# Performance work log

Measured on AMD Instinct MI355X. Metric: run time of the kernel, lower is better.

Reference implementation:

```python
import jax, jax.numpy as jnp
import numpy as np

N_NODES = 50000
N_EDGES = 1000000
IN_F = 128
OUT_F = 128
K = 4
NEG_SLOPE = 0.01  # torch nn.LeakyReLU() default
EPS = 1e-8


def setup_inputs() -> dict:
    key = jax.random.key(0)
    k1, k2, k3, k4, k5, k6 = jax.random.split(key, 6)
    x = jax.random.normal(k1, (N_NODES, IN_F), dtype=jnp.float32)
    e = jax.random.uniform(k2, (N_NODES, K), dtype=jnp.float32)
    stdv = 1.0 / np.sqrt(OUT_F)
    weights = jax.random.uniform(k3, (K, IN_F, OUT_F), minval=-stdv, maxval=stdv, dtype=jnp.float32)
    a = jax.random.normal(k4, (K, 2 * OUT_F, 1), dtype=jnp.float32) * 0.1
    # edge_index with no self-loops (remove_self_loops is then a no-op)
    row = jax.random.randint(k5, (N_EDGES,), 0, N_NODES)
    off = jax.random.randint(k6, (N_EDGES,), 1, N_NODES)
    col = (row + off) % N_NODES
    adj = jnp.stack([row, col]).astype(jnp.int64)
    return {"x": x, "e": e, "weights": weights, "a": a, "adj": adj}


def _canet_gat_forward(x, e, weights, a, adj):
    N = x.shape[0]
    out_f = weights.shape[-1]
    # add self loops (input has none)
    loops = jnp.arange(N, dtype=adj.dtype)
    src = jnp.concatenate([adj[0], loops])  # [Et]
    dst = jnp.concatenate([adj[1], loops])  # [Et]

    # per-head projection: [K, N, O]
    h = jnp.einsum('nd,kdo->kno', x, weights)

    # attention logits: a = [a_src; a_dst], logit_e = leakyrelu(h[src].a_src + h[dst].a_dst)
    a_src = a[:, :out_f, 0]   # [K, O]
    a_dst = a[:, out_f:, 0]   # [K, O]
    s_src = jnp.einsum('kno,ko->kn', h, a_src)  # [K, N]
    s_dst = jnp.einsum('kno,ko->kn', h, a_dst)  # [K, N]
    logits = s_src[:, src] + s_dst[:, dst]      # [K, Et]
    logits = jnp.where(logits >= 0, logits, NEG_SLOPE * logits)
    logits_max = jnp.max(logits, axis=1, keepdims=True)  # global max per head
    edge_e = jnp.exp(logits - logits_max)                # [K, Et]

    outputs = []
    for k in range(h.shape[0]):  # small fixed loop over heads (avoids [K,Et,O] blowup)
        denom = jax.ops.segment_sum(edge_e[k], src, num_segments=N) + EPS   # [N]
        msg = edge_e[k][:, None] * h[k][dst]                                # [Et, O]
        hi_k = jax.ops.segment_sum(msg, src, num_segments=N)                # [N, O]
        outputs.append(hi_k / denom[:, None])
    outputs = jnp.stack(outputs, axis=1)  # [N, K, O]

    out = jnp.sum(e[:, :, None] * outputs, axis=1)  # [N, O]
    return out + x  # residual (in_features == out_features)


def reference(x, e, weights, a, adj):
    return _canet_gat_forward(x, e, weights, a, adj)
```

## Files before the change

### kernel.cpp

```cpp
#include <hip/hip_runtime.h>
#include <hip/hip_bf16.h>
#include <cstddef>

#define NN 50000
#define NE 1000000
#define F  128
#define KH 4
#define NEG 0.01f
#define EPSF 1e-8f
#define CAP 64
#define NBIN 196
#define BINCAP 8192
#define EPB 4096
#define NB1 ((NE + EPB - 1) / EPB)
#define NBW 256
#define NBP 2048
#define STR (NBP * 4)
#define MXSTR 32

typedef short bf16x8 __attribute__((ext_vector_type(8)));
typedef float f32x4 __attribute__((ext_vector_type(4)));

__device__ inline ushort f2bf(float f) {
    __hip_bfloat16 b = __float2bfloat16(f);
    return *reinterpret_cast<ushort*>(&b);
}
__device__ inline float2 bf2_to_f2(unsigned int v) {
    union { unsigned int u; float f; } a, b;
    a.u = (v & 0xffffu) << 16;
    b.u = v & 0xffff0000u;
    return make_float2(a.f, b.f);
}
__device__ inline unsigned int packbf(float xl, float xh) {
    return (unsigned int)f2bf(xl) | ((unsigned int)f2bf(xh) << 16);
}
__device__ inline float lk(float v) { return (v >= 0.f) ? v : NEG * v; }

__global__ __launch_bounds__(256) void bin_kernel(const int* __restrict__ adj,
                                                  int* __restrict__ binTail,
                                                  unsigned int* __restrict__ binbuf,
                                                  const float* __restrict__ W,
                                                  const float* __restrict__ a,
                                                  ushort* __restrict__ wt,
                                                  float* __restrict__ vvg) {
    int b = blockIdx.x;
    int tid = threadIdx.x;
    if (b < NB1) {
        __shared__ int hist[NBIN];
        __shared__ int rpos[NBIN];
        int base = b * EPB;
        int nloc = min(EPB, NE - base);
        for (int i = tid; i < NBIN; i += 256) hist[i] = 0;
        __syncthreads();
        unsigned int pk[16];
#pragma unroll
        for (int u = 0; u < 16; u++) {
            int off = u * 256 + tid;
            if (off < nloc) {
                int e = base + off;
                unsigned int s = (unsigned int)adj[e];
                unsigned int d = (unsigned int)adj[NE + e];
                pk[u] = (s << 16) | d;
                atomicAdd(&hist[s >> 8], 1);
            } else pk[u] = 0xffffffffu;
        }
        __syncthreads();
        for (int i = tid; i < NBIN; i += 256) rpos[i] = atomicAdd(&binTail[i], hist[i]);
        __syncthreads();
#pragma unroll
        for (int u = 0; u < 16; u++) {
            if (pk[u] != 0xffffffffu) {
                int bn = pk[u] >> 24;
                int p = atomicAdd(&rpos[bn], 1);
                if (p < BINCAP) binbuf[(size_t)bn * BINCAP + p] = pk[u];
            }
        }
    } else if (b < NB1 + NBW) {
        int i = (b - NB1) * 256 + tid;
        int k = i >> 14;
        int dd = (i >> 7) & 127;
        int o = i & 127;
        wt[((size_t)k * F + o) * F + dd] = f2bf(W[i]);
    } else {
        int j0 = tid * 4;
#pragma unroll
        for (int ii = 0; ii < 4; ii++) {
            int j = j0 + ii;
            int side = j >> 9;
            int k = (j >> 7) & 3;
            int dd = j & 127;
            const float4* Wr = (const float4*)(W + (size_t)k * F * F + (size_t)dd * F);
            const float4* ar = (const float4*)(a + (size_t)k * 2 * F + side * F);
            float acc = 0.f;
#pragma unroll 8
            for (int o = 0; o < F / 4; o++) {
                float4 wv = Wr[o], av = ar[o];
                acc += wv.x * av.x + wv.y * av.y + wv.z * av.z + wv.w * av.w;
            }
            vvg[j] = acc;
        }
    }
}

__global__ __launch_bounds__(256) void build_prep_kernel(const int* __restrict__ binTail,
                                                         const unsigned int* __restrict__ binbuf,
                                                         int* __restrict__ cnt,
                                                         ushort* __restrict__ bucket16,
                                                         const float* __restrict__ vvg,
                                                         const float* __restrict__ x,
                                                         unsigned int* __restrict__ xb2,
                                                         float* __restrict__ ssrc4,
                                                         float* __restrict__ sdst4,
                                                         int* __restrict__ mxsi) {
    int tid = threadIdx.x;
    __shared__ __align__(16) int shmem[1024];
    __shared__ float bmax_s[4][8];

    if (blockIdx.x < NBIN) {
        int b = blockIdx.x;
        int* lcnt = shmem;
        int* lpos = shmem + 256;
        lcnt[tid] = 0;
        lpos[tid] = 0;
        __syncthreads();
        int tail = min(binTail[b], BINCAP);
        const unsigned int* bb = binbuf + (size_t)b * BINCAP;
        for (int i = tid; i < tail; i += 256) {
            unsigned int pk = bb[i];
            atomicAdd(&lcnt[(pk >> 16) & 255], 1);
        }
        __syncthreads();
        int n0 = b << 8;
        cnt[n0 + tid] = lcnt[tid];
        for (int i = tid; i < tail; i += 256) {
            unsigned int pk = bb[i];
            int sl = (pk >> 16) & 255;
            int p = atomicAdd(&lpos[sl], 1);
            if (p < CAP) bucket16[(size_t)(n0 + sl) * CAP + p] = (ushort)(pk & 0xffffu);
        }
        return;
    }

    float* vvf = (float*)shmem;
    ((float4*)vvf)[tid] = ((const float4*)vvg)[tid];
    __syncthreads();

    int wv = tid >> 6, lane = tid & 63;
    int gw = (blockIdx.x - NBIN) * 4 + wv;
    const float2* x2 = (const float2*)x;
    float2 vs[4], vd[4];
#pragma unroll
    for (int k = 0; k < 4; k++) {
        vs[k] = *(const float2*)&vvf[k * F + 2 * lane];
        vd[k] = *(const float2*)&vvf[(4 + k) * F + 2 * lane];
    }
    int l1 = lane & 1, l2 = lane & 2, l4 = lane & 4;
    int j = 4 * l1 + l2 + (l4 >> 2);
    float* sp = (j < 4) ? (ssrc4 + j) : (sdst4 + (j - 4));
    float mxv = 0.f;

    for (int n = gw; n < NN; n += 2 * STR) {
        int nb = n + STR;
        bool vb = nb < NN;
        float2 xa = x2[(size_t)n * 64 + lane];
        float2 xbv = vb ? x2[(size_t)nb * 64 + lane] : make_float2(0.f, 0.f);
        xb2[(size_t)n * 64 + lane] = packbf(xa.x, xa.y);
        if (vb) xb2[(size_t)nb * 64 + lane] = packbf(xbv.x, xbv.y);
        float s[8], q[8];
#pragma unroll
        for (int k = 0; k < 4; k++) {
            s[k]     = xa.x * vs[k].x + xa.y * vs[k].y;
            s[4 + k] = xa.x * vd[k].x + xa.y * vd[k].y;
            q[k]     = xbv.x * vs[k].x + xbv.y * vs[k].y;
            q[4 + k] = xbv.x * vd[k].x + xbv.y * vd[k].y;
        }
        float tA[4], tB[4];
#pragma unroll
        for (int i = 0; i < 4; i++) {
            float mA = l1 ? s[4 + i] : s[i];
            float oA = __shfl_xor(l1 ? s[i] : s[4 + i], 1);
            tA[i] = mA + oA;
            float mB = l1 ? q[4 + i] : q[i];
            float oB = __shfl_xor(l1 ? q[i] : q[4 + i], 1);
            tB[i] = mB + oB;
        }
        float uA[2], uB[2];
#pragma unroll
        for (int i = 0; i < 2; i++) {
            float mA = l2 ? tA[2 + i] : tA[i];
            float oA = __shfl_xor(l2 ? tA[i] : tA[2 + i], 2);
            uA[i] = mA + oA;
            float mB = l2 ? tB[2 + i] : tB[i];
            float oB = __shfl_xor(l2 ? tB[i] : tB[2 + i], 2);
            uB[i] = mB + oB;
        }
        float vA, vB;
        {
            float mA = l4 ? uA[1] : uA[0];
            float oA = __shfl_xor(l4 ? uA[0] : uA[1], 4);
            vA = mA + oA;
            float mB = l4 ? uB[1] : uB[0];
            float oB = __shfl_xor(l4 ? uB[0] : uB[1], 4);
            vB = mB + oB;
        }
        vA += __shfl_xor(vA, 8);  vB += __shfl_xor(vB, 8);
        vA += __shfl_xor(vA, 16); vB += __shfl_xor(vB, 16);
        vA += __shfl_xor(vA, 32); vB += __shfl_xor(vB, 32);
        if (lane < 8) {
            sp[(size_t)n * 4] = vA;
            if (vb) sp[(size_t)nb * 4] = vB;
        }
        mxv = fmaxf(mxv, fmaxf(vA, vB));
    }
    if (lane < 8) bmax_s[wv][j] = mxv;
    __syncthreads();
    if (tid < 8) {
        float m = fmaxf(fmaxf(bmax_s[0][tid], bmax_s[1][tid]),
                        fmaxf(bmax_s[2][tid], bmax_s[3][tid]));
        atomicMax(&mxsi[tid * MXSTR], __float_as_int(m));
    }
}

__global__ __launch_bounds__(256) void aggregate_kernel(const unsigned int* __restrict__ xb2,
                                                        const float* __restrict__ ssrc4,
                                                        const float* __restrict__ sdst4,
                                                        const float* __restrict__ mxs,
                                                        const int* __restrict__ cnt,
                                                        const ushort* __restrict__ bucket16,
                                                        const float* __restrict__ ew,
                                                        unsigned int* __restrict__ z2) {
    int wv = threadIdx.x >> 6, lane = threadIdx.x & 63;
    int n = blockIdx.x * 4 + wv;
    if (n >= NN) return;

    __shared__ int dsh[4][64];
    __shared__ __align__(16) float wsh[4][64][4];

    float m0 = lk(mxs[0 * MXSTR] + mxs[4 * MXSTR]);
    float m1 = lk(mxs[1 * MXSTR] + mxs[5 * MXSTR]);
    float m2 = lk(mxs[2 * MXSTR] + mxs[6 * MXSTR]);
    float m3 = lk(mxs[3 * MXSTR] + mxs[7 * MXSTR]);
    float4 ss  = *(const float4*)&ssrc4[(size_t)n * 4];
    float4 sdn = *(const float4*)&sdst4[(size_t)n * 4];
    float w0s = __expf(lk(ss.x + sdn.x) - m0);
    float w1s = __expf(lk(ss.y + sdn.y) - m1);
    float w2s = __expf(lk(ss.z + sdn.z) - m2);
    float w3s = __expf(lk(ss.w + sdn.w) - m3);

    int deg = min(cnt[n], CAP);
    if (lane < deg) {
        int d = (int)bucket16[(size_t)n * CAP + lane];
        dsh[wv][lane] = d;
        float4 sd = *(const float4*)&sdst4[(size_t)d * 4];
        float4 w;
        w.x = __expf(lk(ss.x + sd.x) - m0);
        w.y = __expf(lk(ss.y + sd.y) - m1);
        w.z = __expf(lk(ss.z + sd.z) - m2);
        w.w = __expf(lk(ss.w + sd.w) - m3);
        *(float4*)&wsh[wv][lane][0] = w;
    }

    float a0[4], a1[4], den[4];
    {
        float2 f = bf2_to_f2(xb2[(size_t)n * 64 + lane]);
        a0[0] = w0s * f.x; a1[0] = w0s * f.y; den[0] = w0s;
        a0[1] = w1s * f.x; a1[1] = w1s * f.y; den[1] = w1s;
        a0[2] = w2s * f.x; a1[2] = w2s * f.y; den[2] = w2s;
        a0[3] = w3s * f.x; a1[3] = w3s * f.y; den[3] = w3s;
    }

    for (int i = 0; i < deg; i += 8) {
        int du[8]; float4 wu[8]; unsigned int vu[8];
#pragma unroll
        for (int u = 0; u < 8; u++) {
            int iu = i + u;
            bool val = iu < deg;
            int sel = val ? iu : 0;
            du[u] = dsh[wv][sel];
            float4 w = *(const float4*)&wsh[wv][sel][0];
            wu[u] = val ? w : make_float4(0.f, 0.f, 0.f, 0.f);
        }
#pragma unroll
        for (int u = 0; u < 8; u++) vu[u] = xb2[(size_t)du[u] * 64 + lane];
#pragma unroll
        for (int u = 0; u < 8; u++) {
            float2 f = bf2_to_f2(vu[u]);
            float4 w = wu[u];
            a0[0] += w.x * f.x; a1[0] += w.x * f.y; den[0] += w.x;
            a0[1] += w.y * f.x; a1[1] += w.y * f.y; den[1] += w.y;
            a0[2] += w.z * f.x; a1[2] += w.z * f.y; den[2] += w.z;
            a0[3] += w.w * f.x; a1[3] += w.w * f.y; den[3] += w.w;
        }
    }

    float4 e4 = *(const float4*)&ew[(size_t)n * 4];
    float i0 = e4.x / (den[0] + EPSF);
    float i1 = e4.y / (den[1] + EPSF);
    float i2 = e4.z / (den[2] + EPSF);
    float i3 = e4.w / (den[3] + EPSF);
    size_t zb = (size_t)n * 256;
    z2[zb +   0 + lane] = packbf(a0[0] * i0, a1[0] * i0);
    z2[zb +  64 + lane] = packbf(a0[1] * i1, a1[1] * i1);
    z2[zb + 128 + lane] = packbf(a0[2] * i2, a1[2] * i2);
    z2[zb + 192 + lane] = packbf(a0[3] * i3, a1[3] * i3);
}

#define MT 64
__global__ __launch_bounds__(256) void gemm2_kernel(const ushort* __restrict__ z,
                                                    const ushort* __restrict__ wt,
                                                    const float* __restrict__ x,
                                                    float* __restrict__ out) {
    int row0 = blockIdx.x * MT;
    int tid = threadIdx.x;
    int wave = tid >> 6, lane = tid & 63;
    int quad = lane >> 4, l16 = lane & 15;
    __shared__ ushort ws[F][136];

    int arow = row0 + wave * 16 + l16;
    if (arow >= NN) arow = NN - 1;

    f32x4 acc[8];
#pragma unroll
    for (int i = 0; i < 8; i++) acc[i] = (f32x4){0.f, 0.f, 0.f, 0.f};

    for (int k = 0; k < KH; k++) {
        __syncthreads();
        const ushort* wk = wt + (size_t)k * F * F;
        for (int i = tid; i < F * 16; i += 256) {
            int r = i >> 4, c = (i & 15) * 8;
            *(uint4*)&ws[r][c] = *(const uint4*)&wk[r * F + c];
        }
        __syncthreads();
#pragma unroll
        for (int kt = 0; kt < 4; kt++) {
            int kb = kt * 32 + quad * 8;
            bf16x8 af = *(const bf16x8*)&z[(size_t)arow * 512 + k * F + kb];
#pragma unroll
            for (int ni = 0; ni < 8; ni++) {
                bf16x8 bf = *(const bf16x8*)&ws[ni * 16 + l16][kb];
                acc[ni] = __builtin_amdgcn_mfma_f32_16x16x32_bf16(af, bf, acc[ni], 0, 0, 0);
            }
        }
    }
#pragma unroll
    for (int r = 0; r < 4; r++) {
        int n = row0 + wave * 16 + quad * 4 + r;
        if (n < NN) {
#pragma unroll
            for (int ni = 0; ni < 8; ni++) {
                int o = ni * 16 + l16;
                out[(size_t)n * F + o] = x[(size_t)n * F + o] + acc[ni][r];
            }
        }
    }
}

extern "C" void kernel_launch(void* const* d_in, const int* in_sizes, int n_in,
                              void* d_out, int out_size, void* d_ws, size_t ws_size,
                              hipStream_t stream) {
    const float* x = (const float*)d_in[0];
    const float* e = (const float*)d_in[1];
    const float* W = (const float*)d_in[2];
    const float* a = (const float*)d_in[3];
    const int*   adj = (const int*)d_in[4];
    float* out = (float*)d_out;

    char* ws = (char*)d_ws;
    auto take = [&](size_t bytes) {
        char* p = ws;
        ws += (bytes + 255) & ~(size_t)255;
        return p;
    };
    ushort* z      = (ushort*)take((size_t)NN * KH * F * sizeof(ushort));
    unsigned int* xb2 = (unsigned int*)take((size_t)NN * F * sizeof(ushort));
    ushort* wt     = (ushort*)take((size_t)KH * F * F * sizeof(ushort));
    float* ssrc4   = (float*)take((size_t)NN * 4 * sizeof(float));
    float* sdst4   = (float*)take((size_t)NN * 4 * sizeof(float));
    int*   cnt     = (int*)take((size_t)NBIN * 256 * sizeof(int));
    ushort* bucket16 = (ushort*)take((size_t)NBIN * 256 * CAP * sizeof(ushort));
    unsigned int* binbuf = (unsigned int*)take((size_t)NBIN * BINCAP * sizeof(unsigned int));
    int*   binTail = (int*)take((size_t)NBIN * sizeof(int));
    float* mxs     = (float*)take((size_t)8 * MXSTR * sizeof(float));
    float* vvg     = (float*)take((size_t)8 * F * sizeof(float));

    hipMemsetAsync(binTail, 0, (size_t)NBIN * sizeof(int), stream);
    hipMemsetAsync(mxs, 0, (size_t)8 * MXSTR * sizeof(float), stream);
    bin_kernel<<<NB1 + NBW + 1, 256, 0, stream>>>(adj, binTail, binbuf, W, a, wt, vvg);
    build_prep_kernel<<<NBIN + NBP, 256, 0, stream>>>(binTail, binbuf, cnt, bucket16,
                                                      vvg, x, xb2, ssrc4, sdst4, (int*)mxs);
    aggregate_kernel<<<(NN + 3) / 4, 256, 0, stream>>>(xb2, ssrc4, sdst4, mxs, cnt,
                                                       bucket16, e, (unsigned int*)z);
    gemm2_kernel<<<(NN + MT - 1) / MT, 256, 0, stream>>>(z, wt, x, out);
}
```

Measured before the change: 217.8 us.

## Pad bin tail counters, enlarge binning chunks, and streamline aggregate inner loop

The binning kernel now handles 16384 edges per block and reads the adjacency twice instead of holding the packed pairs in registers. The per-bin global tail counters are padded to separate cache lines so fewer atomics contend on the same line. In the aggregate kernel, each wave pads its edge list to a multiple of eight with zero weights, so the per-edge bounds checks go away. It also computes the softmax denominators once with a wave shuffle reduction, and uses readfirstlane to make the neighbour indices scalar for the gathers. The trade-off is fewer, longer-running binning blocks and a second read of the adjacency.

Result: slower. 243.2 us (+11.7%).

```diff
diff --git a/kernel.cpp b/kernel.cpp
--- a/kernel.cpp
+++ b/kernel.cpp
@@ -11,12 +11,13 @@
 #define CAP 64
 #define NBIN 196
 #define BINCAP 8192
-#define EPB 4096
+#define EPB 16384
 #define NB1 ((NE + EPB - 1) / EPB)
 #define NBW 256
 #define NBP 2048
 #define STR (NBP * 4)
 #define MXSTR 32
+#define TSTR 32
 
 typedef short bf16x8 __attribute__((ext_vector_type(8)));
 typedef float f32x4 __attribute__((ext_vector_type(4)));
@@ -24,12 +25,6 @@
 __device__ inline ushort f2bf(float f) {
     __hip_bfloat16 b = __float2bfloat16(f);
     return *reinterpret_cast<ushort*>(&b);
-}
-__device__ inline float2 bf2_to_f2(unsigned int v) {
-    union { unsigned int u; float f; } a, b;
-    a.u = (v & 0xffffu) << 16;
-    b.u = v & 0xffff0000u;
-    return make_float2(a.f, b.f);
 }
 __device__ inline unsigned int packbf(float xl, float xh) {
     return (unsigned int)f2bf(xl) | ((unsigned int)f2bf(xh) << 16);
@@ -47,33 +42,27 @@
     int tid = threadIdx.x;
     if (b < NB1) {
         __shared__ int hist[NBIN];
-        __shared__ int rpos[NBIN];
         int base = b * EPB;
         int nloc = min(EPB, NE - base);
         for (int i = tid; i < NBIN; i += 256) hist[i] = 0;
         __syncthreads();
-        unsigned int pk[16];
-#pragma unroll
-        for (int u = 0; u < 16; u++) {
-            int off = u * 256 + tid;
-            if (off < nloc) {
-                int e = base + off;
-                unsigned int s = (unsigned int)adj[e];
-                unsigned int d = (unsigned int)adj[NE + e];
-                pk[u] = (s << 16) | d;
-                atomicAdd(&hist[s >> 8], 1);
-            } else pk[u] = 0xffffffffu;
-        }
-        __syncthreads();
-        for (int i = tid; i < NBIN; i += 256) rpos[i] = atomicAdd(&binTail[i], hist[i]);
-        __syncthreads();
-#pragma unroll
-        for (int u = 0; u < 16; u++) {
-            if (pk[u] != 0xffffffffu) {
-                int bn = pk[u] >> 24;
-                int p = atomicAdd(&rpos[bn], 1);
-                if (p < BINCAP) binbuf[(size_t)bn * BINCAP + p] = pk[u];
-            }
+        for (int off = tid; off < nloc; off += 256) {
+            unsigned int s = (unsigned int)adj[base + off];
+            atomicAdd(&hist[s >> 8], 1);
+        }
+        __syncthreads();
+        for (int i = tid; i < NBIN; i += 256) {
+            int c = hist[i];
+            hist[i] = atomicAdd(&binTail[i * TSTR], c);
+        }
+        __syncthreads();
+        for (int off = tid; off < nloc; off += 256) {
+            int e = base + off;
+            unsigned int s = (unsigned int)adj[e];
+            unsigned int d = (unsigned int)adj[NE + e];
+            int bn = s >> 8;
+            int p = atomicAdd(&hist[bn], 1);
+            if (p < BINCAP) binbuf[(size_t)bn * BINCAP + p] = (s << 16) | d;
         }
     } else if (b < NB1 + NBW) {
         int i = (b - NB1) * 256 + tid;
@@ -123,7 +112,7 @@
         lcnt[tid] = 0;
         lpos[tid] = 0;
         __syncthreads();
-        int tail = min(binTail[b], BINCAP);
+        int tail = min(binTail[b * TSTR], BINCAP);
         const unsigned int* bb = binbuf + (size_t)b * BINCAP;
         for (int i = tid; i < tail; i += 256) {
             unsigned int pk = bb[i];
@@ -248,56 +237,68 @@
     float w3s = __expf(lk(ss.w + sdn.w) - m3);
 
     int deg = min(cnt[n], CAP);
+    float4 w = make_float4(0.f, 0.f, 0.f, 0.f);
+    int d = 0;
     if (lane < deg) {
-        int d = (int)bucket16[(size_t)n * CAP + lane];
-        dsh[wv][lane] = d;
+        d = (int)bucket16[(size_t)n * CAP + lane];
         float4 sd = *(const float4*)&sdst4[(size_t)d * 4];
-        float4 w;
         w.x = __expf(lk(ss.x + sd.x) - m0);
         w.y = __expf(lk(ss.y + sd.y) - m1);
         w.z = __expf(lk(ss.z + sd.z) - m2);
         w.w = __expf(lk(ss.w + sd.w) - m3);
-        *(float4*)&wsh[wv][lane][0] = w;
-    }
-
-    float a0[4], a1[4], den[4];
+    }
+    dsh[wv][lane] = d;
+    *(float4*)&wsh[wv][lane][0] = w;
+
+    float dn0 = w.x, dn1 = w.y, dn2 = w.z, dn3 = w.w;
+#pragma unroll
+    for (int st = 1; st < 64; st <<= 1) {
+        dn0 += __shfl_xor(dn0, st);
+        dn1 += __shfl_xor(dn1, st);
+        dn2 += __shfl_xor(dn2, st);
+        dn3 += __shfl_xor(dn3, st);
+    }
+
+    float a0[4], a1[4];
     {
-        float2 f = bf2_to_f2(xb2[(size_t)n * 64 + lane]);
-        a0[0] = w0s * f.x; a1[0] = w0s * f.y; den[0] = w0s;
-        a0[1] = w1s * f.x; a1[1] = w1s * f.y; den[1] = w1s;
-        a0[2] = w2s * f.x; a1[2] = w2s * f.y; den[2] = w2s;
-        a0[3] = w3s * f.x; a1[3] = w3s * f.y; den[3] = w3s;
-    }
-
-    for (int i = 0; i < deg; i += 8) {
-        int du[8]; float4 wu[8]; unsigned int vu[8];
+        unsigned int v = xb2[(size_t)n * 64 + lane];
+        union { unsigned int u; float f; } lo, hi;
+        lo.u = v << 16;
+        hi.u = v & 0xffff0000u;
+        a0[0] = w0s * lo.f; a1[0] = w0s * hi.f;
+        a0[1] = w1s * lo.f; a1[1] = w1s * hi.f;
+        a0[2] = w2s * lo.f; a1[2] = w2s * hi.f;
+        a0[3] = w3s * lo.f; a1[3] = w3s * hi.f;
+    }
+
+    int degp = (deg + 7) & ~7;
+    for (int i = 0; i < degp; i += 8) {
+        int du[8];
+#pragma unroll
+        for (int u = 0; u < 8; u++)
+            du[u] = __builtin_amdgcn_readfirstlane(dsh[wv][i + u]);
+        unsigned int vu[8];
+#pragma unroll
+        for (int u = 0; u < 8; u++)
+            vu[u] = xb2[(size_t)du[u] * 64 + lane];
 #pragma unroll
         for (int u = 0; u < 8; u++) {
-            int iu = i + u;
-            bool val = iu < deg;
-            int sel = val ? iu : 0;
-            du[u] = dsh[wv][sel];
-            float4 w = *(const float4*)&wsh[wv][sel][0];
-            wu[u] = val ? w : make_float4(0.f, 0.f, 0.f, 0.f);
-        }
-#pragma unroll
-        for (int u = 0; u < 8; u++) vu[u] = xb2[(size_t)du[u] * 64 + lane];
-#pragma unroll
-        for (int u = 0; u < 8; u++) {
-            float2 f = bf2_to_f2(vu[u]);
-            float4 w = wu[u];
-            a0[0] += w.x * f.x; a1[0] += w.x * f.y; den[0] += w.x;
-            a0[1] += w.y * f.x; a1[1] += w.y * f.y; den[1] += w.y;
-            a0[2] += w.z * f.x; a1[2] += w.z * f.y; den[2] += w.z;
-            a0[3] += w.w * f.x; a1[3] += w.w * f.y; den[3] += w.w;
+            float4 w4 = *(const float4*)&wsh[wv][i + u][0];
+            union { unsigned int uu; float f; } lo, hi;
+            lo.uu = vu[u] << 16;
+            hi.uu = vu[u] & 0xffff0000u;
+            a0[0] += w4.x * lo.f; a1[0] += w4.x * hi.f;
+            a0[1] += w4.y * lo.f; a1[1] += w4.y * hi.f;
+            a0[2] += w4.z * lo.f; a1[2] += w4.z * hi.f;
+            a0[3] += w4.w * lo.f; a1[3] += w4.w * hi.f;
         }
     }
 
     float4 e4 = *(const float4*)&ew[(size_t)n * 4];
-    float i0 = e4.x / (den[0] + EPSF);
-    float i1 = e4.y / (den[1] + EPSF);
-    float i2 = e4.z / (den[2] + EPSF);
-    float i3 = e4.w / (den[3] + EPSF);
+    float i0 = e4.x / (w0s + dn0 + EPSF);
+    float i1 = e4.y / (w1s + dn1 + EPSF);
+    float i2 = e4.z / (w2s + dn2 + EPSF);
+    float i3 = e4.w / (w3s + dn3 + EPSF);
     size_t zb = (size_t)n * 256;
     z2[zb +   0 + lane] = packbf(a0[0] * i0, a1[0] * i0);
     z2[zb +  64 + lane] = packbf(a0[1] * i1, a1[1] * i1);
@@ -379,11 +380,11 @@
     int*   cnt     = (int*)take((size_t)NBIN * 256 * sizeof(int));
     ushort* bucket16 = (ushort*)take((size_t)NBIN * 256 * CAP * sizeof(ushort));
     unsigned int* binbuf = (unsigned int*)take((size_t)NBIN * BINCAP * sizeof(unsigned int));
-    int*   binTail = (int*)take((size_t)NBIN * sizeof(int));
+    int*   binTail = (int*)take((size_t)NBIN * TSTR * sizeof(int));
     float* mxs     = (float*)take((size_t)8 * MXSTR * sizeof(float));
     float* vvg     = (float*)take((size_t)8 * F * sizeof(float));
 
-    hipMemsetAsync(binTail, 0, (size_t)NBIN * sizeof(int), stream);
+    hipMemsetAsync(binTail, 0, (size_t)NBIN * TSTR * sizeof(int), stream);
     hipMemsetAsync(mxs, 0, (size_t)8 * MXSTR * sizeof(float), stream);
     bin_kernel<<<NB1 + NBW + 1, 256, 0, stream>>>(adj, binTail, binbuf, W, a, wt, vvg);
     build_prep_kernel<<<NBIN + NBP, 256, 0, stream>>>(binTail, binbuf, cnt, bucket16,
```
